# Performance work log

Hardware: AMD Instinct MI355X
Metric: run time of the kernel (lower is better)

The kernel has to match this reference:

```python
import jax, jax.numpy as jnp
import numpy as np

SPATIAL_PATH = np.array([[1,0,1],[0,1,2],[1,2,1],[4,3,1],[5,4,3],[6,5,4],[5,6,5],[8,7,1],[9,8,7],[10,9,8],[9,10,9]], dtype=np.int32)

B, C_IN, J, T, C_OUT = 64, 3, 11, 512, 128
TEMPORAL_LEN = 7
SIG_CH = 84  # c = C_IN + 1 = 4 -> 4 + 16 + 64


def _signature_depth3(path):
    """Depth-3 path signature with basepoint=0 (Chen's identity over exp of increments).
    path: [N, L, c] -> [N, c + c^2 + c^3]."""
    N, L, c = path.shape
    # basepoint=True: path starts at 0, so first increment is path[:, 0]
    inc = jnp.concatenate([path[:, :1], path[:, 1:] - path[:, :-1]], axis=1)  # [N, L, c]

    def step(carry, d):
        S1, S2, S3 = carry
        e2 = 0.5 * d[:, :, None] * d[:, None, :]                                  # d^{x2}/2!
        e3 = (d[:, :, None, None] * d[:, None, :, None] * d[:, None, None, :]) / 6.0  # d^{x3}/3!
        T1 = S1 + d
        T2 = S2 + S1[:, :, None] * d[:, None, :] + e2
        T3 = (S3 + S2[:, :, :, None] * d[:, None, None, :]
              + S1[:, :, None, None] * e2[:, None, :, :] + e3)
        return (T1, T2, T3), None

    z = lambda *s: jnp.zeros(s, path.dtype)
    (S1, S2, S3), _ = jax.lax.scan(step, (z(N, c), z(N, c, c), z(N, c, c, c)),
                                   jnp.swapaxes(inc, 0, 1))
    return jnp.concatenate([S1, S2.reshape(N, -1), S3.reshape(N, -1)], axis=1)


def _augment_time(path):
    # signatory.Augment(include_time=True, include_original=True): prepend linear time channel
    N, L, _ = path.shape
    t = jnp.broadcast_to(jnp.linspace(0.0, 1.0, L, dtype=path.dtype)[None, :, None], (N, L, 1))
    return jnp.concatenate([t, path], axis=-1)


def _bn(x, gamma, beta, eps=1e-5):
    # train-mode BatchNorm2d (batch statistics), matching module default mode
    m = x.mean(axis=(0, 2, 3), keepdims=True)
    v = x.var(axis=(0, 2, 3), keepdims=True)
    return (x - m) * jax.lax.rsqrt(v + eps) * gamma[None, :, None, None] + beta[None, :, None, None]


def _conv1x1(x, w, b):
    return jnp.einsum('bcjt,oc->bojt', x, w) + b[None, :, None, None]


def _forward(x, path, raw_w, raw_b, raw_g, raw_beta,
             ps_w, ps_b, ps_g, ps_beta, fus_w, fus_b, fus_g, fus_beta):
    B_, C, J_, T_ = x.shape
    # raw branch: Conv2d(C_in, C_out, (1,3), pad (0,1)) + BN + ReLU
    x_conv = jax.lax.conv_general_dilated(x, raw_w, (1, 1), [(0, 0), (1, 1)],
                                          dimension_numbers=('NCHW', 'OIHW', 'NCHW'))
    x_conv = jax.nn.relu(_bn(x_conv + raw_b[None, :, None, None], raw_g, raw_beta))

    # spatial joint paths: gather along joint dim with hand-crafted path [J, 3]
    xp = x.transpose(0, 1, 3, 2)                  # [B, C, T, J]
    sp = xp[:, :, :, path]                        # [B, C, T, J, 3]
    sp = sp.transpose(0, 2, 3, 4, 1).reshape(-1, path.shape[1], C)  # [B*T*J, 3, C]
    s_sig = _signature_depth3(_augment_time(sp))
    s_sig = s_sig.reshape(B_, T_, J_, SIG_CH).transpose(0, 3, 2, 1)  # [B, 84, J, T]

    # temporal paths: replicate-pad T and take 7-wide sliding windows per joint
    pad = (TEMPORAL_LEN - 1) // 2
    x_pad = jnp.pad(x, ((0, 0), (0, 0), (0, 0), (pad, pad)), mode='edge')
    widx = jnp.arange(T_)[:, None] + jnp.arange(TEMPORAL_LEN)[None, :]  # [T, 7]
    tp = x_pad[:, :, :, widx]                     # [B, C, J, T, 7]
    tp = tp.transpose(0, 3, 2, 4, 1).reshape(-1, TEMPORAL_LEN, C)       # [B*T*J, 7, C]
    t_sig = _signature_depth3(_augment_time(tp))
    t_sig = t_sig.reshape(B_, T_, J_, SIG_CH).transpose(0, 3, 2, 1)     # [B, 84, J, T]

    sig = jnp.concatenate([s_sig, t_sig], axis=1)                       # [B, 168, J, T]
    sig = jax.nn.relu(_bn(_conv1x1(sig, ps_w, ps_b), ps_g, ps_beta))    # [B, C_out, J, T]

    out = jnp.concatenate([x_conv, sig], axis=1)                        # [B, 2*C_out, J, T]
    return jax.nn.relu(_bn(_conv1x1(out, fus_w, fus_b), fus_g, fus_beta))


def setup_inputs() -> dict:
    key = jax.random.key(0)
    ks = jax.random.split(key, 4)
    return {
        'x': jax.random.normal(ks[0], (B, C_IN, J, T), jnp.float32),
        'path': jnp.asarray(SPATIAL_PATH),
        'raw_w': jax.random.normal(ks[1], (C_OUT, C_IN, 1, 3), jnp.float32) * 0.2,
        'raw_b': jnp.zeros((C_OUT,), jnp.float32),
        'raw_g': jnp.ones((C_OUT,), jnp.float32),
        'raw_beta': jnp.zeros((C_OUT,), jnp.float32),
        'ps_w': jax.random.normal(ks[2], (C_OUT, 2 * SIG_CH), jnp.float32) * 0.05,
        'ps_b': jnp.zeros((C_OUT,), jnp.float32),
        'ps_g': jnp.ones((C_OUT,), jnp.float32),
        'ps_beta': jnp.zeros((C_OUT,), jnp.float32),
        'fus_w': jax.random.normal(ks[3], (C_OUT, 2 * C_OUT), jnp.float32) * 0.05,
        'fus_b': jnp.zeros((C_OUT,), jnp.float32),
        'fus_g': jnp.ones((C_OUT,), jnp.float32),
        'fus_beta': jnp.zeros((C_OUT,), jnp.float32),
    }


def reference(x, path, raw_w, raw_b, raw_g, raw_beta, ps_w, ps_b, ps_g, ps_beta,
              fus_w, fus_b, fus_g, fus_beta):
    return _forward(x, path, raw_w, raw_b, raw_g, raw_beta,
                    ps_w, ps_b, ps_g, ps_beta, fus_w, fus_b, fus_g, fus_beta)
```

## Files before the change

### kernel.cpp

```cpp
#include <hip/hip_runtime.h>

#define B_    64
#define CIN_  3
#define J_    11
#define T_    512
#define CO_   128
#define KPS_  168
#define KPAD_ 192
#define NLOC_ (B_*J_*T_)
#define NSTATF_ 360448.0f

typedef unsigned short u16;
typedef unsigned int   u32;

typedef __attribute__((ext_vector_type(8))) short bh8;
typedef __attribute__((ext_vector_type(4))) float f32x4;

__device__ __forceinline__ float b2f(u16 u){ union{u32 i; float f;} v; v.i = ((u32)u)<<16; return v.f; }
__device__ __forceinline__ u16 f2b(float f){ union{float f; u32 i;} v; v.f=f; u32 r = v.i + 0x7FFFu + ((v.i>>16)&1u); return (u16)(r>>16); }
__device__ __forceinline__ u32 pk2(u16 a, u16 b){ return (u32)a | ((u32)b<<16); }

template<bool BF>
__device__ __forceinline__ float ldx(const void* p, size_t i){
  if constexpr (BF) return b2f(((const u16*)p)[i]);
  else              return ((const float*)p)[i];
}

__global__ void kdet(const u32* __restrict__ xw, u32* __restrict__ flag){
  __shared__ int cnt;
  if (threadIdx.x==0) cnt=0;
  __syncthreads();
  u32 w = xw[threadIdx.x*4 + 1];
  int e = (int)((w>>7)&0xFFu);
  if (e>=100 && e<=140) atomicAdd(&cnt,1);
  __syncthreads();
  if (threadIdx.x==0) *flag = (cnt>128) ? 1u : 0u;
}

__global__ __launch_bounds__(256) void k0a_zero(float* __restrict__ statsY, float* __restrict__ statsF){
  const int stride = gridDim.x*blockDim.x;
  const int t0 = blockIdx.x*blockDim.x + threadIdx.x;
  for (int i=t0;i<64*512;i+=stride) statsY[i]=0.f;
  for (int i=t0;i<64*256;i+=stride) statsF[i]=0.f;
}

template<bool BF>
__global__ __launch_bounds__(256) void k0b_tr(const u32* __restrict__ flag,
    const void* __restrict__ ps_w, const void* __restrict__ fus_w,
    u16* __restrict__ psB, u16* __restrict__ fusB)
{
  if (*flag != (BF?1u:0u)) return;
  const int stride = gridDim.x*blockDim.x;
  const int t0 = blockIdx.x*blockDim.x + threadIdx.x;
  for (int i=t0;i<128*KPAD_;i+=stride){
    int o=i/KPAD_, kk=i-o*KPAD_;
    int k = (kk<84) ? kk : ((kk>=96 && kk<180) ? kk-12 : -1);
    psB[i] = (k>=0) ? f2b(ldx<BF>(ps_w, (size_t)o*KPS_+k)) : (u16)0;
  }
  for (int i=t0;i<128*256;i+=stride){
    int o=i>>8, k=i&255;
    int kc=k>>6, kk=k&63;
    int byte=(o<<7)+(kk<<1); byte ^= ((o&7)<<4);
    fusB[(kc*16384 + byte)>>1] = f2b(ldx<BF>(fus_w,i));
  }
}

__device__ __forceinline__ void sigstep(float* S1, float* S2, float* S3, const float* d){
  float e2[16];
  #pragma unroll
  for (int a=0;a<4;a++){
    #pragma unroll
    for (int b=0;b<4;b++) e2[a*4+b] = 0.5f*d[a]*d[b];
  }
  #pragma unroll
  for (int a=0;a<4;a++){
    float s1e = S1[a] + (1.0f/3.0f)*d[a];
    #pragma unroll
    for (int b=0;b<4;b++){
      #pragma unroll
      for (int c=0;c<4;c++){
        S3[a*16+b*4+c] += S2[a*4+b]*d[c] + s1e*e2[b*4+c];
      }
    }
  }
  #pragma unroll
  for (int a=0;a<4;a++){
    #pragma unroll
    for (int b=0;b<4;b++) S2[a*4+b] += S1[a]*d[b] + e2[a*4+b];
  }
  #pragma unroll
  for (int a=0;a<4;a++) S1[a] += d[a];
}

template<bool BF>
__global__ __launch_bounds__(256) void k1_sig_conv(const u32* __restrict__ flag,
    const void* __restrict__ x, const int* __restrict__ path,
    const void* __restrict__ raw_w, const void* __restrict__ raw_b,
    const void* __restrict__ ps_b, const u16* __restrict__ psB,
    u16* __restrict__ Y, float* __restrict__ statsY,
    int locOff, int writeY, int doStats)
{
  if (*flag != (BF?1u:0u)) return;
  __shared__ u16 sAhi[64*KPAD_];
  __shared__ u16 sAlo[64*KPAD_];
  __shared__ float xt[CIN_][72];
  __shared__ float xs[CIN_][3][64];
  __shared__ int   pj[3];

  const int tid = threadIdx.x;
  const int blk = blockIdx.x;
  const int lb  = locOff + blk*64;
  const int lbl = blk*64;
  const int b   = lb / (J_*T_);
  const int j   = (lb / T_) % J_;
  const int t0  = lb % T_;
  const size_t xbase = (size_t)b*CIN_*J_*T_;

  if (tid < 3) pj[tid] = path[j*3 + tid];
  for (int idx=tid; idx<CIN_*70; idx+=256){
    int c=idx/70, u=idx-c*70;
    int t=t0+u-3; t = t<0?0:(t>T_-1?T_-1:t);
    xt[c][u] = ldx<BF>(x, xbase + (size_t)(c*J_+j)*T_ + t);
  }
  __syncthreads();
  for (int idx=tid; idx<CIN_*3*64; idx+=256){
    int c=idx/192, p=(idx>>6)%3, tt=idx&63;
    xs[c][p][tt] = ldx<BF>(x, xbase + (size_t)(c*J_+pj[p])*T_ + t0 + tt);
  }
  __syncthreads();

  const int lane = tid & 63, wid = tid >> 6;
  const int wid2 = wid ^ ((blk&1)<<1);

  if (wid2 < 2){
    const bool spf = (wid2==0);
    const int  tt  = lane;
    const int  L   = spf ? 3 : 7;
    const float dt = spf ? 0.5f : (1.0f/6.0f);
    float S1[4], S2[16], S3[64];
    #pragma unroll
    for (int i=0;i<4;i++)  S1[i]=0.f;
    #pragma unroll
    for (int i=0;i<16;i++) S2[i]=0.f;
    #pragma unroll
    for (int i=0;i<64;i++) S3[i]=0.f;
    float prv[3], d[4];
    for (int c=0;c<3;c++) prv[c] = spf ? xs[c][0][tt] : xt[c][tt];
    d[0]=0.f; d[1]=prv[0]; d[2]=prv[1]; d[3]=prv[2];
    sigstep(S1,S2,S3,d);
    for (int s=1;s<L;s++){
      d[0]=dt;
      for (int c=0;c<3;c++){ float cv = spf ? xs[c][s][tt] : xt[c][tt+s]; d[c+1]=cv-prv[c]; prv[c]=cv; }
      sigstep(S1,S2,S3,d);
    }
    const int sb2 = spf ? 0 : 192;
    const int rowb = tt*(KPAD_*2);
    const int swz  = (tt&7)<<4;
    #pragma unroll
    for (int i=0;i<12;i++){
      u16 hv[8], lv[8];
      #pragma unroll
      for (int e=0;e<8;e++){
        const int idx = i*8+e;
        float v;
        if (idx<4) v=S1[idx]; else if (idx<20) v=S2[idx-4]; else if (idx<84) v=S3[idx-20]; else v=0.f;
        u16 h = f2b(v);
        hv[e]=h; lv[e]=f2b(v - b2f(h));
      }
      int byp = (rowb + sb2 + i*16) ^ swz;
      *reinterpret_cast<uint4*>((char*)sAhi + byp) =
          make_uint4(pk2(hv[0],hv[1]),pk2(hv[2],hv[3]),pk2(hv[4],hv[5]),pk2(hv[6],hv[7]));
      *reinterpret_cast<uint4*>((char*)sAlo + byp) =
          make_uint4(pk2(lv[0],lv[1]),pk2(lv[2],lv[3]),pk2(lv[4],lv[5]),pk2(lv[6],lv[7]));
    }
  } else {
    const int nid = (wid2-2)*64 + lane;
    const int tx = nid & 7, ty2 = nid >> 3;
    #pragma unroll
    for (int cg=0; cg<2; cg++){
      const int chb = cg*64 + ty2*4;
      float w[4][9], bia[4];
      #pragma unroll
      for (int c=0;c<4;c++){
        bia[c]=ldx<BF>(raw_b, chb+c);
        #pragma unroll
        for (int q=0;q<9;q++) w[c][q]=ldx<BF>(raw_w, (size_t)(chb+c)*9+q);
      }
      float accC[8][4];
      #pragma unroll
      for (int i=0;i<8;i++){
        const int tl=tx*8+i, tg=t0+tl;
        float xv[9];
        #pragma unroll
        for (int cc=0;cc<3;cc++){
          #pragma unroll
          for (int kt=0;kt<3;kt++){
            float v = xt[cc][tl+2+kt];
            if ((tg==0 && kt==0) || (tg==T_-1 && kt==2)) v=0.f;
            xv[cc*3+kt]=v;
          }
        }
        #pragma unroll
        for (int c=0;c<4;c++){
          float s=bia[c];
          #pragma unroll
          for (int q=0;q<9;q++) s=fmaf(xv[q],w[c][q],s);
          accC[i][c]=s;
        }
      }
      if (writeY){
        #pragma unroll
        for (int i=0;i<8;i++){
          u16* yp = Y + (size_t)(lbl + tx*8+i)*256 + chb;
          *reinterpret_cast<uint2*>(yp) =
            make_uint2(pk2(f2b(accC[i][0]),f2b(accC[i][1])), pk2(f2b(accC[i][2]),f2b(accC[i][3])));
        }
      }
      if (doStats){
        #pragma unroll
        for (int c=0;c<4;c++){
          float s=0.f,q=0.f;
          #pragma unroll
          for (int i=0;i<8;i++){ float v=accC[i][c]; s+=v; q+=v*v; }
          s += __shfl_xor(s,1); s += __shfl_xor(s,2); s += __shfl_xor(s,4);
          q += __shfl_xor(q,1); q += __shfl_xor(q,2); q += __shfl_xor(q,4);
          if ((lane&7)==0){
            atomicAdd(&statsY[(blk&63)*512 + (chb+c)*2 + 0], s);
            atomicAdd(&statsY[(blk&63)*512 + (chb+c)*2 + 1], q);
          }
        }
      }
    }
  }
  __syncthreads();

  const int lrow = lane >> 4, lcol = lane & 15;
  f32x4 acc[2][4];
  #pragma unroll
  for (int mt=0;mt<2;mt++)
    #pragma unroll
    for (int nt=0;nt<4;nt++) acc[mt][nt] = (f32x4){0.f,0.f,0.f,0.f};

  #pragma unroll
  for (int ks=0;ks<6;ks++){
    const int kk2 = ks*64 + lrow*16;
    bh8 wf[2], yh[4], yl[4];
    #pragma unroll
    for (int mt=0;mt<2;mt++){
      const int o = wid*32 + mt*16 + lcol;
      wf[mt] = *reinterpret_cast<const bh8*>((const char*)psB + o*(KPAD_*2) + kk2);
    }
    #pragma unroll
    for (int nt=0;nt<4;nt++){
      const int l = nt*16 + lcol;
      const int byp = (l*(KPAD_*2) + kk2) ^ ((l&7)<<4);
      yh[nt] = *reinterpret_cast<const bh8*>((const char*)sAhi + byp);
      yl[nt] = *reinterpret_cast<const bh8*>((const char*)sAlo + byp);
    }
    #pragma unroll
    for (int mt=0;mt<2;mt++){
      #pragma unroll
      for (int nt=0;nt<4;nt++){
        acc[mt][nt] = __builtin_amdgcn_mfma_f32_16x16x32_bf16(wf[mt], yh[nt], acc[mt][nt], 0,0,0);
        acc[mt][nt] = __builtin_amdgcn_mfma_f32_16x16x32_bf16(wf[mt], yl[nt], acc[mt][nt], 0,0,0);
      }
    }
  }

  #pragma unroll
  for (int mt=0;mt<2;mt++){
    const int chb = wid*32 + mt*16 + lrow*4;
    float pb[4];
    #pragma unroll
    for (int r=0;r<4;r++) pb[r]=ldx<BF>(ps_b, chb+r);
    float sv[4]={0.f,0.f,0.f,0.f}, qv[4]={0.f,0.f,0.f,0.f};
    #pragma unroll
    for (int nt=0;nt<4;nt++){
      float v0=acc[mt][nt][0]+pb[0], v1=acc[mt][nt][1]+pb[1];
      float v2=acc[mt][nt][2]+pb[2], v3=acc[mt][nt][3]+pb[3];
      sv[0]+=v0; qv[0]+=v0*v0; sv[1]+=v1; qv[1]+=v1*v1;
      sv[2]+=v2; qv[2]+=v2*v2; sv[3]+=v3; qv[3]+=v3*v3;
      if (writeY){
        u16* yp = Y + (size_t)(lbl + nt*16+lcol)*256 + 128 + chb;
        *reinterpret_cast<uint2*>(yp) = make_uint2(pk2(f2b(v0),f2b(v1)), pk2(f2b(v2),f2b(v3)));
      }
    }
    if (doStats){
      #pragma unroll
      for (int r=0;r<4;r++){
        float s=sv[r], q=qv[r];
        s += __shfl_xor(s,1); s += __shfl_xor(s,2); s += __shfl_xor(s,4); s += __shfl_xor(s,8);
        q += __shfl_xor(q,1); q += __shfl_xor(q,2); q += __shfl_xor(q,4); q += __shfl_xor(q,8);
        if (lcol==0){
          const int ch = 128 + chb + r;
          atomicAdd(&statsY[(blk&63)*512 + ch*2 + 0], s);
          atomicAdd(&statsY[(blk&63)*512 + ch*2 + 1], q);
        }
      }
    }
  }
}

template<bool BF>
__global__ __launch_bounds__(256) void k2_finY(const u32* __restrict__ flag,
    const float* __restrict__ statsY,
    const void* __restrict__ raw_g, const void* __restrict__ raw_beta,
    const void* __restrict__ ps_g,  const void* __restrict__ ps_beta,
    float* __restrict__ scaleY, float* __restrict__ shiftY)
{
  if (*flag != (BF?1u:0u)) return;
  int ch = threadIdx.x;
  float s=0.f,q=0.f;
  for (int slot=0;slot<64;slot++){ s+=statsY[slot*512+ch*2]; q+=statsY[slot*512+ch*2+1]; }
  float m = s/NSTATF_;
  float v = q/NSTATF_ - m*m; v = fmaxf(v,0.f);
  float r = rsqrtf(v + 1e-5f);
  float g  = (ch<128)? ldx<BF>(raw_g,ch)    : ldx<BF>(ps_g,ch-128);
  float be = (ch<128)? ldx<BF>(raw_beta,ch) : ldx<BF>(ps_beta,ch-128);
  scaleY[ch]=r*g; shiftY[ch]=be - m*r*g;
}

template<bool BF>
__global__ __launch_bounds__(256,4) void k3_fus(const u32* __restrict__ flag,
    const u16* __restrict__ Y,
    const u16* __restrict__ fusB, const float* __restrict__ scaleY, const float* __restrict__ shiftY,
    const void* __restrict__ fus_b, void* __restrict__ F, float* __restrict__ statsF,
    int locOff)
{
  if (*flag != (BF?1u:0u)) return;
  __shared__ u16 sAhi[128*64];
  __shared__ u16 sB  [128*64];
  __shared__ float sSc[256], sSh[256];

  const int tid = threadIdx.x, blk = blockIdx.x;
  const size_t loc0  = (size_t)locOff + (size_t)blk*128;
  const size_t loc0l = (size_t)blk*128;
  const int lane = tid & 63, wid = tid >> 6;
  const int wm = wid >> 1, wn = wid & 1;
  const int lrow = lane >> 4, lcol = lane & 15;

  sSc[tid] = scaleY[tid];
  sSh[tid] = shiftY[tid];

  f32x4 acc[4][4];
  #pragma unroll
  for (int mt=0;mt<4;mt++)
    #pragma unroll
    for (int nt=0;nt<4;nt++) acc[mt][nt] = (f32x4){0.f,0.f,0.f,0.f};

  __syncthreads();

  for (int kc=0;kc<4;kc++){
    const int kb = kc*64;
    #pragma unroll
    for (int p=0;p<4;p++){
      const int loc = p*32 + (tid>>3);
      const int c16 = tid & 7;
      const int ch0 = kb + c16*8;
      uint4 u = *reinterpret_cast<const uint4*>(Y + (loc0l+loc)*256 + ch0);
      float f[8];
      f[0]=b2f((u16)(u.x&0xffff)); f[1]=b2f((u16)(u.x>>16));
      f[2]=b2f((u16)(u.y&0xffff)); f[3]=b2f((u16)(u.y>>16));
      f[4]=b2f((u16)(u.z&0xffff)); f[5]=b2f((u16)(u.z>>16));
      f[6]=b2f((u16)(u.w&0xffff)); f[7]=b2f((u16)(u.w>>16));
      u16 hi[8];
      #pragma unroll
      for (int jq=0;jq<8;jq++){
        float v = fmaxf(fmaf(f[jq], sSc[ch0+jq], sSh[ch0+jq]), 0.f);
        hi[jq] = f2b(v);
      }
      int byte = (loc<<7) + (c16<<4); byte ^= ((loc&7)<<4);
      *reinterpret_cast<uint4*>((char*)sAhi + byte) =
          make_uint4(pk2(hi[0],hi[1]),pk2(hi[2],hi[3]),pk2(hi[4],hi[5]),pk2(hi[6],hi[7]));
    }
    {
      const char* src = (const char*)(fusB + kc*8192);
      #pragma unroll
      for (int p=0;p<4;p++){
        int q16 = (p*256 + tid) << 4;
        *reinterpret_cast<uint4*>((char*)sB + q16) =
            *reinterpret_cast<const uint4*>(src + q16);
      }
    }
    __syncthreads();
    #pragma unroll
    for (int ks=0;ks<2;ks++){
      const int kk2 = (ks*32 + lrow*8) << 1;
      bh8 wf[4], yh[4];
      #pragma unroll
      for (int mt=0;mt<4;mt++){
        int o = wm*64 + mt*16 + lcol;
        int byp = (o<<7) + kk2; byp ^= ((o&7)<<4);
        wf[mt] = *reinterpret_cast<const bh8*>((const char*)sB + byp);
      }
      #pragma unroll
      for (int nt=0;nt<4;nt++){
        int l = wn*64 + nt*16 + lcol;
        int byp = (l<<7) + kk2; byp ^= ((l&7)<<4);
        yh[nt] = *reinterpret_cast<const bh8*>((const char*)sAhi + byp);
      }
      #pragma unroll
      for (int mt=0;mt<4;mt++){
        #pragma unroll
        for (int nt=0;nt<4;nt++){
          acc[mt][nt] = __builtin_amdgcn_mfma_f32_16x16x32_bf16(wf[mt], yh[nt], acc[mt][nt], 0,0,0);
        }
      }
    }
    __syncthreads();
  }

  const int bb  = (int)(loc0/(J_*T_));
  const int jj  = (int)((loc0/T_)%J_);
  const int tt0 = (int)(loc0%T_);
  #pragma unroll
  for (int mt=0;mt<4;mt++){
    #pragma unroll
    for (int r=0;r<4;r++){
      const int ch = wm*64 + mt*16 + lrow*4 + r;
      const float fb = ldx<BF>(fus_b, ch);
      const size_t ro = ((size_t)(bb*128+ch)*J_ + jj)*T_ + tt0 + wn*64 + lcol;
      float s=0.f, q=0.f;
      #pragma unroll
      for (int nt=0;nt<4;nt++){
        float v = acc[mt][nt][r] + fb;
        s += v; q += v*v;
        if constexpr (BF){
          float vp = __shfl_xor(v, 1);
          if (!(lane&1)){
            *reinterpret_cast<u32*>((u16*)F + ro + nt*16) = pk2(f2b(v), f2b(vp));
          }
        } else {
          ((float*)F)[ro + nt*16] = v;
        }
      }
      s += __shfl_xor(s,1); s += __shfl_xor(s,2); s += __shfl_xor(s,4); s += __shfl_xor(s,8);
      q += __shfl_xor(q,1); q += __shfl_xor(q,2); q += __shfl_xor(q,4); q += __shfl_xor(q,8);
      if (lcol==0){
        atomicAdd(&statsF[(blk&63)*256 + ch*2 + 0], s);
        atomicAdd(&statsF[(blk&63)*256 + ch*2 + 1], q);
      }
    }
  }
}

template<bool BF>
__global__ __launch_bounds__(256) void k4_finF(const u32* __restrict__ flag,
    const float* __restrict__ statsF,
    const void* __restrict__ fus_g, const void* __restrict__ fus_beta,
    float* __restrict__ scaleF, float* __restrict__ shiftF)
{
  if (*flag != (BF?1u:0u)) return;
  int ch = threadIdx.x;
  if (ch < 128){
    float s=0.f,q=0.f;
    for (int slot=0;slot<64;slot++){ s+=statsF[slot*256+ch*2]; q+=statsF[slot*256+ch*2+1]; }
    float m=s/NSTATF_;
    float v=fmaxf(q/NSTATF_-m*m,0.f);
    float r=rsqrtf(v+1e-5f);
    float g=ldx<BF>(fus_g,ch), be=ldx<BF>(fus_beta,ch);
    scaleF[ch]=r*g; shiftF[ch]=be - m*r*g;
  }
}

template<bool BF>
__global__ __launch_bounds__(256) void k5_out(const u32* __restrict__ flag,
    const float* __restrict__ scaleF, const float* __restrict__ shiftF, void* __restrict__ out)
{
  if (*flag != (BF?1u:0u)) return;
  if constexpr (BF){
    size_t idx = ((size_t)blockIdx.x*256 + threadIdx.x)*8;
    int ch = (int)((idx/(J_*T_)) & 127);
    float sc = scaleF[ch], sh = shiftF[ch];
    u16* o16 = (u16*)out;
    uint4 u = *reinterpret_cast<const uint4*>(o16 + idx);
    u32 w[4] = {u.x,u.y,u.z,u.w};
    u32 o[4];
    #pragma unroll
    for (int q=0;q<4;q++){
      float v0=fmaxf(fmaf(b2f((u16)(w[q]&0xffff)),sc,sh),0.f);
      float v1=fmaxf(fmaf(b2f((u16)(w[q]>>16)),sc,sh),0.f);
      o[q]=pk2(f2b(v0),f2b(v1));
    }
    *reinterpret_cast<uint4*>(o16 + idx) = make_uint4(o[0],o[1],o[2],o[3]);
  } else {
    size_t idx = ((size_t)blockIdx.x*256 + threadIdx.x)*4;
    int ch = (int)((idx/(J_*T_)) & 127);
    float sc = scaleF[ch], sh = shiftF[ch];
    float* of = (float*)out;
    float4 v = *reinterpret_cast<const float4*>(of + idx);
    v.x=fmaxf(fmaf(v.x,sc,sh),0.f);
    v.y=fmaxf(fmaf(v.y,sc,sh),0.f);
    v.z=fmaxf(fmaf(v.z,sc,sh),0.f);
    v.w=fmaxf(fmaf(v.w,sc,sh),0.f);
    *reinterpret_cast<float4*>(of + idx) = v;
  }
}

extern "C" void kernel_launch(void* const* d_in, const int* in_sizes, int n_in,
                              void* d_out, int out_size, void* d_ws, size_t ws_size,
                              hipStream_t stream)
{
  const void* x        = d_in[0];
  const int*  path     = (const int*)d_in[1];
  const void* raw_w    = d_in[2];
  const void* raw_b    = d_in[3];
  const void* raw_g    = d_in[4];
  const void* raw_beta = d_in[5];
  const void* ps_w     = d_in[6];
  const void* ps_b     = d_in[7];
  const void* ps_g     = d_in[8];
  const void* ps_beta  = d_in[9];
  const void* fus_w    = d_in[10];
  const void* fus_b    = d_in[11];
  const void* fus_g    = d_in[12];
  const void* fus_beta = d_in[13];

  char* w = (char*)d_ws;
  u32*   flag   = (u32*)w;   w += 256;
  float* statsY = (float*)w; w += 64*512*4;
  float* statsF = (float*)w; w += 64*256*4;
  u16*   psB    = (u16*)w;   w += 128*KPAD_*2;
  u16*   fusB   = (u16*)w;   w += 256*128*2;
  float* scaleY = (float*)w; w += 1024;
  float* shiftY = (float*)w; w += 1024;
  float* scaleF = (float*)w; w += 512;
  float* shiftF = (float*)w; w += 512;
  size_t off = (size_t)(w - (char*)d_ws);
  off = (off + 255) & ~(size_t)255;
  u16* Y = (u16*)((char*)d_ws + off);
  size_t avail = (ws_size > off) ? (ws_size - off) : 0;

  const size_t Yfull = (size_t)NLOC_*256*2;
  int c = 1;
  while (c < 64 && Yfull/(size_t)c > avail) c <<= 1;
  const int chunkLoc = NLOC_ / c;

  kdet<<<dim3(1),dim3(256),0,stream>>>((const u32*)x, flag);
  k0a_zero<<<dim3(64),dim3(256),0,stream>>>(statsY, statsF);
  k0b_tr<false><<<dim3(64),dim3(256),0,stream>>>(flag, ps_w, fus_w, psB, fusB);
  k0b_tr<true ><<<dim3(64),dim3(256),0,stream>>>(flag, ps_w, fus_w, psB, fusB);

  for (int i=0;i<c;i++){
    int wy = (i==c-1)?1:0;
    k1_sig_conv<false><<<dim3(chunkLoc/64),dim3(256),0,stream>>>(flag, x, path, raw_w, raw_b, ps_b, psB, Y, statsY, i*chunkLoc, wy, 1);
    k1_sig_conv<true ><<<dim3(chunkLoc/64),dim3(256),0,stream>>>(flag, x, path, raw_w, raw_b, ps_b, psB, Y, statsY, i*chunkLoc, wy, 1);
  }
  k2_finY<false><<<dim3(1),dim3(256),0,stream>>>(flag, statsY, raw_g, raw_beta, ps_g, ps_beta, scaleY, shiftY);
  k2_finY<true ><<<dim3(1),dim3(256),0,stream>>>(flag, statsY, raw_g, raw_beta, ps_g, ps_beta, scaleY, shiftY);

  k3_fus<false><<<dim3(chunkLoc/128),dim3(256),0,stream>>>(flag, Y, fusB, scaleY, shiftY, fus_b, d_out, statsF, (c-1)*chunkLoc);
  k3_fus<true ><<<dim3(chunkLoc/128),dim3(256),0,stream>>>(flag, Y, fusB, scaleY, shiftY, fus_b, d_out, statsF, (c-1)*chunkLoc);
  for (int i=0;i<c-1;i++){
    k1_sig_conv<false><<<dim3(chunkLoc/64),dim3(256),0,stream>>>(flag, x, path, raw_w, raw_b, ps_b, psB, Y, statsY, i*chunkLoc, 1, 0);
    k1_sig_conv<true ><<<dim3(chunkLoc/64),dim3(256),0,stream>>>(flag, x, path, raw_w, raw_b, ps_b, psB, Y, statsY, i*chunkLoc, 1, 0);
    k3_fus<false><<<dim3(chunkLoc/128),dim3(256),0,stream>>>(flag, Y, fusB, scaleY, shiftY, fus_b, d_out, statsF, i*chunkLoc);
    k3_fus<true ><<<dim3(chunkLoc/128),dim3(256),0,stream>>>(flag, Y, fusB, scaleY, shiftY, fus_b, d_out, statsF, i*chunkLoc);
  }
  k4_finF<false><<<dim3(1),dim3(256),0,stream>>>(flag, statsF, fus_g, fus_beta, scaleF, shiftF);
  k4_finF<true ><<<dim3(1),dim3(256),0,stream>>>(flag, statsF, fus_g, fus_beta, scaleF, shiftF);
  k5_out<false><<<dim3(NLOC_*128/(256*4)),dim3(256),0,stream>>>(flag, scaleF, shiftF, d_out);
  k5_out<true ><<<dim3(NLOC_*128/(256*8)),dim3(256),0,stream>>>(flag, scaleF, shiftF, d_out);
}
```

Measured before the change: 535.5 us.

## Merge dtype-templated kernel pairs into runtime-flag kernels and stage Y stores via LDS

Replaces each pair of dtype-specialised kernel launches (fp32 and bf16, one of which exits early) with a single kernel that reads the dtype flag at runtime through readfirstlane. It also merges the zeroing and weight-transpose prep kernels into one. The PS-branch Y output is now staged through swizzled shared memory and written with coalesced 16-byte stores instead of scattered 8-byte stores, and k5_out becomes a grid-stride loop over 2048 blocks. The aim is to cut launch count and empty-block overhead and improve store coalescing, at the cost of runtime branches and extra barriers inside the kernels.

```diff
diff --git a/kernel.cpp b/kernel.cpp
--- a/kernel.cpp
+++ b/kernel.cpp
@@ -20,10 +20,12 @@
 __device__ __forceinline__ u16 f2b(float f){ union{float f; u32 i;} v; v.f=f; u32 r = v.i + 0x7FFFu + ((v.i>>16)&1u); return (u16)(r>>16); }
 __device__ __forceinline__ u32 pk2(u16 a, u16 b){ return (u32)a | ((u32)b<<16); }
 
-template<bool BF>
-__device__ __forceinline__ float ldx(const void* p, size_t i){
-  if constexpr (BF) return b2f(((const u16*)p)[i]);
-  else              return ((const float*)p)[i];
+__device__ __forceinline__ float ldx(const void* p, size_t i, bool bf){
+  if (bf) return b2f(((const u16*)p)[i]);
+  return ((const float*)p)[i];
+}
+__device__ __forceinline__ bool rflag(const u32* flag){
+  return __builtin_amdgcn_readfirstlane(*flag) != 0u;
 }
 
 __global__ void kdet(const u32* __restrict__ xw, u32* __restrict__ flag){
@@ -37,31 +39,26 @@
   if (threadIdx.x==0) *flag = (cnt>128) ? 1u : 0u;
 }
 
-__global__ __launch_bounds__(256) void k0a_zero(float* __restrict__ statsY, float* __restrict__ statsF){
+__global__ __launch_bounds__(256) void k0_prep(const u32* __restrict__ flag,
+    const void* __restrict__ ps_w, const void* __restrict__ fus_w,
+    u16* __restrict__ psB, u16* __restrict__ fusB,
+    float* __restrict__ statsY, float* __restrict__ statsF)
+{
+  const bool bf = rflag(flag);
   const int stride = gridDim.x*blockDim.x;
   const int t0 = blockIdx.x*blockDim.x + threadIdx.x;
   for (int i=t0;i<64*512;i+=stride) statsY[i]=0.f;
   for (int i=t0;i<64*256;i+=stride) statsF[i]=0.f;
-}
-
-template<bool BF>
-__global__ __launch_bounds__(256) void k0b_tr(const u32* __restrict__ flag,
-    const void* __restrict__ ps_w, const void* __restrict__ fus_w,
-    u16* __restrict__ psB, u16* __restrict__ fusB)
-{
-  if (*flag != (BF?1u:0u)) return;
-  const int stride = gridDim.x*blockDim.x;
-  const int t0 = blockIdx.x*blockDim.x + threadIdx.x;
   for (int i=t0;i<128*KPAD_;i+=stride){
     int o=i/KPAD_, kk=i-o*KPAD_;
     int k = (kk<84) ? kk : ((kk>=96 && kk<180) ? kk-12 : -1);
-    psB[i] = (k>=0) ? f2b(ldx<BF>(ps_w, (size_t)o*KPS_+k)) : (u16)0;
+    psB[i] = (k>=0) ? f2b(ldx(ps_w, (size_t)o*KPS_+k, bf)) : (u16)0;
   }
   for (int i=t0;i<128*256;i+=stride){
     int o=i>>8, k=i&255;
     int kc=k>>6, kk=k&63;
     int byte=(o<<7)+(kk<<1); byte ^= ((o&7)<<4);
-    fusB[(kc*16384 + byte)>>1] = f2b(ldx<BF>(fus_w,i));
+    fusB[(kc*16384 + byte)>>1] = f2b(ldx(fus_w,i,bf));
   }
 }
 
@@ -92,7 +89,6 @@
   for (int a=0;a<4;a++) S1[a] += d[a];
 }
 
-template<bool BF>
 __global__ __launch_bounds__(256) void k1_sig_conv(const u32* __restrict__ flag,
     const void* __restrict__ x, const int* __restrict__ path,
     const void* __restrict__ raw_w, const void* __restrict__ raw_b,
@@ -100,7 +96,7 @@
     u16* __restrict__ Y, float* __restrict__ statsY,
     int locOff, int writeY, int doStats)
 {
-  if (*flag != (BF?1u:0u)) return;
+  const bool bf = rflag(flag);
   __shared__ u16 sAhi[64*KPAD_];
   __shared__ u16 sAlo[64*KPAD_];
   __shared__ float xt[CIN_][72];
@@ -120,12 +116,12 @@
   for (int idx=tid; idx<CIN_*70; idx+=256){
     int c=idx/70, u=idx-c*70;
     int t=t0+u-3; t = t<0?0:(t>T_-1?T_-1:t);
-    xt[c][u] = ldx<BF>(x, xbase + (size_t)(c*J_+j)*T_ + t);
+    xt[c][u] = ldx(x, xbase + (size_t)(c*J_+j)*T_ + t, bf);
   }
   __syncthreads();
   for (int idx=tid; idx<CIN_*3*64; idx+=256){
     int c=idx/192, p=(idx>>6)%3, tt=idx&63;
-    xs[c][p][tt] = ldx<BF>(x, xbase + (size_t)(c*J_+pj[p])*T_ + t0 + tt);
+    xs[c][p][tt] = ldx(x, xbase + (size_t)(c*J_+pj[p])*T_ + t0 + tt, bf);
   }
   __syncthreads();
 
@@ -182,9 +178,9 @@
       float w[4][9], bia[4];
       #pragma unroll
       for (int c=0;c<4;c++){
-        bia[c]=ldx<BF>(raw_b, chb+c);
+        bia[c]=ldx(raw_b, chb+c, bf);
         #pragma unroll
-        for (int q=0;q<9;q++) w[c][q]=ldx<BF>(raw_w, (size_t)(chb+c)*9+q);
+        for (int q=0;q<9;q++) w[c][q]=ldx(raw_w, (size_t)(chb+c)*9+q, bf);
       }
       float accC[8][4];
       #pragma unroll
@@ -266,23 +262,27 @@
       }
     }
   }
-
+  __syncthreads();
+
+  char* yPs = (char*)sAhi;
   #pragma unroll
   for (int mt=0;mt<2;mt++){
     const int chb = wid*32 + mt*16 + lrow*4;
     float pb[4];
     #pragma unroll
-    for (int r=0;r<4;r++) pb[r]=ldx<BF>(ps_b, chb+r);
+    for (int r=0;r<4;r++) pb[r]=ldx(ps_b, chb+r, bf);
     float sv[4]={0.f,0.f,0.f,0.f}, qv[4]={0.f,0.f,0.f,0.f};
     #pragma unroll
     for (int nt=0;nt<4;nt++){
+      const int loc = nt*16 + lcol;
       float v0=acc[mt][nt][0]+pb[0], v1=acc[mt][nt][1]+pb[1];
       float v2=acc[mt][nt][2]+pb[2], v3=acc[mt][nt][3]+pb[3];
       sv[0]+=v0; qv[0]+=v0*v0; sv[1]+=v1; qv[1]+=v1*v1;
       sv[2]+=v2; qv[2]+=v2*v2; sv[3]+=v3; qv[3]+=v3*v3;
       if (writeY){
-        u16* yp = Y + (size_t)(lbl + nt*16+lcol)*256 + 128 + chb;
-        *reinterpret_cast<uint2*>(yp) = make_uint2(pk2(f2b(v0),f2b(v1)), pk2(f2b(v2),f2b(v3)));
+        const int byp = (loc*256 + chb*2) ^ ((loc&7)<<4);
+        *reinterpret_cast<uint2*>(yPs + byp) =
+            make_uint2(pk2(f2b(v0),f2b(v1)), pk2(f2b(v2),f2b(v3)));
       }
     }
     if (doStats){
@@ -299,35 +299,45 @@
       }
     }
   }
-}
-
-template<bool BF>
+  __syncthreads();
+  if (writeY){
+    #pragma unroll
+    for (int it=0; it<4; it++){
+      const int q = it*256 + tid;
+      const int L = q<<4;
+      const int loc = L>>8;
+      const int phys = L ^ ((loc&7)<<4);
+      uint4 v = *reinterpret_cast<const uint4*>(yPs + phys);
+      *reinterpret_cast<uint4*>((char*)Y + ((size_t)(lbl+loc)<<9) + 256 + (L&255)) = v;
+    }
+  }
+}
+
 __global__ __launch_bounds__(256) void k2_finY(const u32* __restrict__ flag,
     const float* __restrict__ statsY,
     const void* __restrict__ raw_g, const void* __restrict__ raw_beta,
     const void* __restrict__ ps_g,  const void* __restrict__ ps_beta,
     float* __restrict__ scaleY, float* __restrict__ shiftY)
 {
-  if (*flag != (BF?1u:0u)) return;
+  const bool bf = rflag(flag);
   int ch = threadIdx.x;
   float s=0.f,q=0.f;
   for (int slot=0;slot<64;slot++){ s+=statsY[slot*512+ch*2]; q+=statsY[slot*512+ch*2+1]; }
   float m = s/NSTATF_;
   float v = q/NSTATF_ - m*m; v = fmaxf(v,0.f);
   float r = rsqrtf(v + 1e-5f);
-  float g  = (ch<128)? ldx<BF>(raw_g,ch)    : ldx<BF>(ps_g,ch-128);
-  float be = (ch<128)? ldx<BF>(raw_beta,ch) : ldx<BF>(ps_beta,ch-128);
+  float g  = (ch<128)? ldx(raw_g,ch,bf)    : ldx(ps_g,ch-128,bf);
+  float be = (ch<128)? ldx(raw_beta,ch,bf) : ldx(ps_beta,ch-128,bf);
   scaleY[ch]=r*g; shiftY[ch]=be - m*r*g;
 }
 
-template<bool BF>
 __global__ __launch_bounds__(256,4) void k3_fus(const u32* __restrict__ flag,
     const u16* __restrict__ Y,
     const u16* __restrict__ fusB, const float* __restrict__ scaleY, const float* __restrict__ shiftY,
     const void* __restrict__ fus_b, void* __restrict__ F, float* __restrict__ statsF,
     int locOff)
 {
-  if (*flag != (BF?1u:0u)) return;
+  const bool bf = rflag(flag);
   __shared__ u16 sAhi[128*64];
   __shared__ u16 sB  [128*64];
   __shared__ float sSc[256], sSh[256];
@@ -418,15 +428,15 @@
     #pragma unroll
     for (int r=0;r<4;r++){
       const int ch = wm*64 + mt*16 + lrow*4 + r;
-      const float fb = ldx<BF>(fus_b, ch);
+      const float fb = ldx(fus_b, ch, bf);
       const size_t ro = ((size_t)(bb*128+ch)*J_ + jj)*T_ + tt0 + wn*64 + lcol;
       float s=0.f, q=0.f;
       #pragma unroll
       for (int nt=0;nt<4;nt++){
         float v = acc[mt][nt][r] + fb;
         s += v; q += v*v;
-        if constexpr (BF){
-          float vp = __shfl_xor(v, 1);
+        float vp = __shfl_xor(v, 1);
+        if (bf){
           if (!(lane&1)){
             *reinterpret_cast<u32*>((u16*)F + ro + nt*16) = pk2(f2b(v), f2b(vp));
           }
@@ -444,13 +454,12 @@
   }
 }
 
-template<bool BF>
 __global__ __launch_bounds__(256) void k4_finF(const u32* __restrict__ flag,
     const float* __restrict__ statsF,
     const void* __restrict__ fus_g, const void* __restrict__ fus_beta,
     float* __restrict__ scaleF, float* __restrict__ shiftF)
 {
-  if (*flag != (BF?1u:0u)) return;
+  const bool bf = rflag(flag);
   int ch = threadIdx.x;
   if (ch < 128){
     float s=0.f,q=0.f;
@@ -458,42 +467,47 @@
     float m=s/NSTATF_;
     float v=fmaxf(q/NSTATF_-m*m,0.f);
     float r=rsqrtf(v+1e-5f);
-    float g=ldx<BF>(fus_g,ch), be=ldx<BF>(fus_beta,ch);
+    float g=ldx(fus_g,ch,bf), be=ldx(fus_beta,ch,bf);
     scaleF[ch]=r*g; shiftF[ch]=be - m*r*g;
   }
 }
 
-template<bool BF>
 __global__ __launch_bounds__(256) void k5_out(const u32* __restrict__ flag,
     const float* __restrict__ scaleF, const float* __restrict__ shiftF, void* __restrict__ out)
 {
-  if (*flag != (BF?1u:0u)) return;
-  if constexpr (BF){
-    size_t idx = ((size_t)blockIdx.x*256 + threadIdx.x)*8;
-    int ch = (int)((idx/(J_*T_)) & 127);
-    float sc = scaleF[ch], sh = shiftF[ch];
+  const bool bf = rflag(flag);
+  const size_t total = (size_t)NLOC_*128;
+  const size_t stride = (size_t)gridDim.x*blockDim.x;
+  if (bf){
     u16* o16 = (u16*)out;
-    uint4 u = *reinterpret_cast<const uint4*>(o16 + idx);
-    u32 w[4] = {u.x,u.y,u.z,u.w};
-    u32 o[4];
-    #pragma unroll
-    for (int q=0;q<4;q++){
-      float v0=fmaxf(fmaf(b2f((u16)(w[q]&0xffff)),sc,sh),0.f);
-      float v1=fmaxf(fmaf(b2f((u16)(w[q]>>16)),sc,sh),0.f);
-      o[q]=pk2(f2b(v0),f2b(v1));
-    }
-    *reinterpret_cast<uint4*>(o16 + idx) = make_uint4(o[0],o[1],o[2],o[3]);
+    for (size_t u8 = (size_t)blockIdx.x*blockDim.x + threadIdx.x; u8*8 < total; u8 += stride){
+      size_t idx = u8*8;
+      int ch = (int)((idx/(J_*T_)) & 127);
+      float sc = scaleF[ch], sh = shiftF[ch];
+      uint4 u = *reinterpret_cast<const uint4*>(o16 + idx);
+      u32 w[4] = {u.x,u.y,u.z,u.w};
+      u32 o[4];
+      #pragma unroll
+      for (int q=0;q<4;q++){
+        float v0=fmaxf(fmaf(b2f((u16)(w[q]&0xffff)),sc,sh),0.f);
+        float v1=fmaxf(fmaf(b2f((u16)(w[q]>>16)),sc,sh),0.f);
+        o[q]=pk2(f2b(v0),f2b(v1));
+      }
+      *reinterpret_cast<uint4*>(o16 + idx) = make_uint4(o[0],o[1],o[2],o[3]);
+    }
   } else {
-    size_t idx = ((size_t)blockIdx.x*256 + threadIdx.x)*4;
-    int ch = (int)((idx/(J_*T_)) & 127);
-    float sc = scaleF[ch], sh = shiftF[ch];
     float* of = (float*)out;
-    float4 v = *reinterpret_cast<const float4*>(of + idx);
-    v.x=fmaxf(fmaf(v.x,sc,sh),0.f);
-    v.y=fmaxf(fmaf(v.y,sc,sh),0.f);
-    v.z=fmaxf(fmaf(v.z,sc,sh),0.f);
-    v.w=fmaxf(fmaf(v.w,sc,sh),0.f);
-    *reinterpret_cast<float4*>(of + idx) = v;
+    for (size_t u4 = (size_t)blockIdx.x*blockDim.x + threadIdx.x; u4*4 < total; u4 += stride){
+      size_t idx = u4*4;
+      int ch = (int)((idx/(J_*T_)) & 127);
+      float sc = scaleF[ch], sh = shiftF[ch];
+      float4 v = *reinterpret_cast<const float4*>(of + idx);
+      v.x=fmaxf(fmaf(v.x,sc,sh),0.f);
+      v.y=fmaxf(fmaf(v.y,sc,sh),0.f);
+      v.z=fmaxf(fmaf(v.z,sc,sh),0.f);
+      v.w=fmaxf(fmaf(v.w,sc,sh),0.f);
+      *reinterpret_cast<float4*>(of + idx) = v;
+    }
   }
 }
 
@@ -537,28 +551,19 @@
   const int chunkLoc = NLOC_ / c;
 
   kdet<<<dim3(1),dim3(256),0,stream>>>((const u32*)x, flag);
-  k0a_zero<<<dim3(64),dim3(256),0,stream>>>(statsY, statsF);
-  k0b_tr<false><<<dim3(64),dim3(256),0,stream>>>(flag, ps_w, fus_w, psB, fusB);
-  k0b_tr<true ><<<dim3(64),dim3(256),0,stream>>>(flag, ps_w, fus_w, psB, fusB);
+  k0_prep<<<dim3(64),dim3(256),0,stream>>>(flag, ps_w, fus_w, psB, fusB, statsY, statsF);
 
   for (int i=0;i<c;i++){
     int wy = (i==c-1)?1:0;
-    k1_sig_conv<false><<<dim3(chunkLoc/64),dim3(256),0,stream>>>(flag, x, path, raw_w, raw_b, ps_b, psB, Y, statsY, i*chunkLoc, wy, 1);
-    k1_sig_conv<true ><<<dim3(chunkLoc/64),dim3(256),0,stream>>>(flag, x, path, raw_w, raw_b, ps_b, psB, Y, statsY, i*chunkLoc, wy, 1);
-  }
-  k2_finY<false><<<dim3(1),dim3(256),0,stream>>>(flag, statsY, raw_g, raw_beta, ps_g, ps_beta, scaleY, shiftY);
-  k2_finY<true ><<<dim3(1),dim3(256),0,stream>>>(flag, statsY, raw_g, raw_beta, ps_g, ps_beta, scaleY, shiftY);
-
-  k3_fus<false><<<dim3(chunkLoc/128),dim3(256),0,stream>>>(flag, Y, fusB, scaleY, shiftY, fus_b, d_out, statsF, (c-1)*chunkLoc);
-  k3_fus<true ><<<dim3(chunkLoc/128),dim3(256),0,stream>>>(flag, Y, fusB, scaleY, shiftY, fus_b, d_out, statsF, (c-1)*chunkLoc);
+    k1_sig_conv<<<dim3(chunkLoc/64),dim3(256),0,stream>>>(flag, x, path, raw_w, raw_b, ps_b, psB, Y, statsY, i*chunkLoc, wy, 1);
+  }
+  k2_finY<<<dim3(1),dim3(256),0,stream>>>(flag, statsY, raw_g, raw_beta, ps_g, ps_beta, scaleY, shiftY);
+
+  k3_fus<<<dim3(chunkLoc/128),dim3(256),0,stream>>>(flag, Y, fusB, scaleY, shiftY, fus_b, d_out, statsF, (c-1)*chunkLoc);
   for (int i=0;i<c-1;i++){
-    k1_sig_conv<false><<<dim3(chunkLoc/64),dim3(256),0,stream>>>(flag, x, path, raw_w, raw_b, ps_b, psB, Y, statsY, i*chunkLoc, 1, 0);
-    k1_sig_conv<true ><<<dim3(chunkLoc/64),dim3(256),0,stream>>>(flag, x, path, raw_w, raw_b, ps_b, psB, Y, statsY, i*chunkLoc, 1, 0);
-    k3_fus<false><<<dim3(chunkLoc/128),dim3(256),0,stream>>>(flag, Y, fusB, scaleY, shiftY, fus_b, d_out, statsF, i*chunkLoc);
-    k3_fus<true ><<<dim3(chunkLoc/128),dim3(256),0,stream>>>(flag, Y, fusB, scaleY, shiftY, fus_b, d_out, statsF, i*chunkLoc);
-  }
-  k4_finF<false><<<dim3(1),dim3(256),0,stream>>>(flag, statsF, fus_g, fus_beta, scaleF, shiftF);
-  k4_finF<true ><<<dim3(1),dim3(256),0,stream>>>(flag, statsF, fus_g, fus_beta, scaleF, shiftF);
-  k5_out<false><<<dim3(NLOC_*128/(256*4)),dim3(256),0,stream>>>(flag, scaleF, shiftF, d_out);
-  k5_out<true ><<<dim3(NLOC_*128/(256*8)),dim3(256),0,stream>>>(flag, scaleF, shiftF, d_out);
-}
+    k1_sig_conv<<<dim3(chunkLoc/64),dim3(256),0,stream>>>(flag, x, path, raw_w, raw_b, ps_b, psB, Y, statsY, i*chunkLoc, 1, 0);
+    k3_fus<<<dim3(chunkLoc/128),dim3(256),0,stream>>>(flag, Y, fusB, scaleY, shiftY, fus_b, d_out, statsF, i*chunkLoc);
+  }
+  k4_finF<<<dim3(1),dim3(256),0,stream>>>(flag, statsF, fus_g, fus_beta, scaleF, shiftF);
+  k5_out<<<dim3(2048),dim3(256),0,stream>>>(flag, scaleF, shiftF, d_out);
+}
```

After: 551.3 us. +3.0%, slower.
